# Optimization experiments

Measured on AMD Instinct MI355X. Metric: run time of the kernel, lower is better.

## Reference

```python
import jax, jax.numpy as jnp
from jax import lax
import numpy as np

K = 31      # avg_pool2d kernel_size
PAD = 15    # avg_pool2d padding
EPS = 1.0
GAMMA = 5.0


def _box_avg(x):
    # Separable 31x31 box filter, stride 1, zero padding 15,
    # count_include_pad=True (PyTorch default) -> always divide by K*K.
    s = lax.reduce_window(x, 0.0, lax.add, (1, 1, K, 1), (1, 1, 1, 1),
                          [(0, 0), (0, 0), (PAD, PAD), (0, 0)])
    s = lax.reduce_window(s, 0.0, lax.add, (1, 1, 1, K), (1, 1, 1, 1),
                          [(0, 0), (0, 0), (0, 0), (PAD, PAD)])
    return s / (K * K)


def setup_inputs() -> dict:
    key = jax.random.key(0)
    k1, k2 = jax.random.split(key)
    shape = (64, 1, 512, 512)  # [B, C, H, W]
    inp = jax.random.uniform(k1, shape, dtype=jnp.float32)
    tgt = jax.random.uniform(k2, shape, dtype=jnp.float32)
    return {"input": inp, "target": tgt}


def reference(input, target):
    weight = 1.0 + GAMMA * jnp.abs(_box_avg(target) - target)
    intersection = jnp.sum(input * target * weight)
    denom = jnp.sum(input * weight) + jnp.sum(target * weight)
    dice = (2.0 * intersection + EPS) / (denom + EPS)
    return 1.0 - dice
```

## Files before the change

### kernel.cpp

```cpp
#include <hip/hip_runtime.h>
#include <hip/hip_bf16.h>


#define BATCH 64
#define H     512
#define W     512
#define PADR  15
#define RBAND 32
#define RING  38
#define NBLK  (BATCH * (H / RBAND))

static __device__ __forceinline__ unsigned pack2(float e, float o) {
    __hip_bfloat162 h = __float22bfloat162_rn(make_float2(e, o));
    unsigned u; __builtin_memcpy(&u, &h, 4); return u;
}
static __device__ __forceinline__ float2 unpk(unsigned u) {
    return make_float2(__uint_as_float(u << 16),
                       __uint_as_float(u & 0xffff0000u));
}

__global__ __launch_bounds__(256, 4) void fused_kernel(const float* __restrict__ tgt,
                                                       const float* __restrict__ inp,
                                                       float4* __restrict__ partials) {
    const int tid  = threadIdx.x;
    const int lane = tid & 63;
    const int wv   = tid >> 6;
    const int blk  = blockIdx.x;
    const int band = blk & 15;
    const int b    = blk >> 4;
    const int R0   = band * RBAND;
    const float* timg = tgt + (size_t)b * H * W;
    const float* iimg = inp + (size_t)b * H * W;

    __shared__ __align__(16) unsigned ring[RING * 256];

    const int col0 = lane * 8;
    const int ofs  = lane * 4;

    for (int k = 0; k < 10; ++k) {
        const int r_off = wv + 4 * k;
        if (r_off < RING) {
            const int row = R0 - 15 + r_off;
            float4 v0 = make_float4(0.f, 0.f, 0.f, 0.f), v1 = v0;
            if (row >= 0) {
                v0 = *(const float4*)(timg + (size_t)row * W + col0);
                v1 = *(const float4*)(timg + (size_t)row * W + col0 + 4);
            }
            uint4 u;
            u.x = pack2(v0.x, v0.y); u.y = pack2(v0.z, v0.w);
            u.z = pack2(v1.x, v1.y); u.w = pack2(v1.z, v1.w);
            *(uint4*)&ring[((row + RING) % RING) * 256 + ofs] = u;
        }
    }
    __syncthreads();

    const float mL1 = (lane >= 1) ? 1.f : 0.f;
    const float mR1 = (lane <= 62) ? 1.f : 0.f;
    const float mL2 = (lane >= 2) ? 1.f : 0.f;
    const float mR2 = (lane <= 61) ? 1.f : 0.f;

    float vr[8];
    #pragma unroll
    for (int k = 0; k < 8; ++k) vr[k] = 0.f;
    #pragma unroll
    for (int jj = -PADR; jj <= PADR; ++jj) {
        const int rr = R0 + wv + jj;
        const uint4 c = *(const uint4*)&ring[((rr + RING) % RING) * 256 + ofs];
        const float2 e0 = unpk(c.x), e1 = unpk(c.y), e2 = unpk(c.z), e3 = unpk(c.w);
        vr[0] += e0.x; vr[1] += e0.y; vr[2] += e1.x; vr[3] += e1.y;
        vr[4] += e2.x; vr[5] += e2.y; vr[6] += e3.x; vr[7] += e3.y;
    }

    const float inv = 1.0f / 961.0f;
    float aI = 0.f, aA = 0.f, aB = 0.f;

    for (int j = 0; j < 8; ++j) {
        const int h = R0 + 4 * j + wv;

        float4 pf0 = make_float4(0.f, 0.f, 0.f, 0.f), pf1 = pf0;
        const int prow = R0 + 4 * j + 23 + wv;
        if (j < 7 && prow < H) {
            pf0 = *(const float4*)(timg + (size_t)prow * W + col0);
            pf1 = *(const float4*)(timg + (size_t)prow * W + col0 + 4);
        }
        const float4 i0 = *(const float4*)(iimg + (size_t)h * W + col0);
        const float4 i1 = *(const float4*)(iimg + (size_t)h * W + col0 + 4);

        const uint4 tc = *(const uint4*)&ring[(h % RING) * 256 + ofs];

        uint4 ua[4], us[4];
        if (j < 7) {
            #pragma unroll
            for (int q = 0; q < 4; ++q) {
                const int ar = h + 16 + q;
                ua[q] = (ar < H) ? *(const uint4*)&ring[(ar % RING) * 256 + ofs]
                                 : make_uint4(0u, 0u, 0u, 0u);
                us[q] = *(const uint4*)&ring[(((h - 15 + q) + RING) % RING) * 256 + ofs];
            }
        }

        const float p1 = vr[0];
        const float p2 = p1 + vr[1];
        const float p3 = p2 + vr[2];
        const float p4 = p3 + vr[3];
        const float p5 = p4 + vr[4];
        const float p6 = p5 + vr[5];
        const float p7 = p6 + vr[6];
        const float s  = p7 + vr[7];
        const float f1 = s - p1, f2 = s - p2, f3 = s - p3, f4 = s - p4;
        const float f5 = s - p5, f6 = s - p6, f7 = s - p7;

        const float sL1 = __shfl_up(s, 1, 64);
        const float sR1 = __shfl_down(s, 1, 64);
        const float g1 = __shfl_up(f1, 2, 64);
        const float g2 = __shfl_up(f2, 2, 64);
        const float g3 = __shfl_up(f3, 2, 64);
        const float g4 = __shfl_up(f4, 2, 64);
        const float g5 = __shfl_up(f5, 2, 64);
        const float g6 = __shfl_up(f6, 2, 64);
        const float g7 = __shfl_up(f7, 2, 64);
        const float q1 = __shfl_down(p1, 2, 64);
        const float q2 = __shfl_down(p2, 2, 64);
        const float q3 = __shfl_down(p3, 2, 64);
        const float q4 = __shfl_down(p4, 2, 64);
        const float q5 = __shfl_down(p5, 2, 64);
        const float q6 = __shfl_down(p6, 2, 64);
        const float q7 = __shfl_down(p7, 2, 64);

        const float S3 = fmaf(mL1, sL1, fmaf(mR1, sR1, s));
        float win[8];
        win[0] = fmaf(mL2, g1, S3);
        win[1] = fmaf(mL2, g2, fmaf(mR2, q1, S3));
        win[2] = fmaf(mL2, g3, fmaf(mR2, q2, S3));
        win[3] = fmaf(mL2, g4, fmaf(mR2, q3, S3));
        win[4] = fmaf(mL2, g5, fmaf(mR2, q4, S3));
        win[5] = fmaf(mL2, g6, fmaf(mR2, q5, S3));
        win[6] = fmaf(mL2, g7, fmaf(mR2, q6, S3));
        win[7] = fmaf(mR2, q7, S3);

        const float2 t0 = unpk(tc.x), t1 = unpk(tc.y), t2 = unpk(tc.z), t3 = unpk(tc.w);
        const float tv[8] = {t0.x, t0.y, t1.x, t1.y, t2.x, t2.y, t3.x, t3.y};
        const float iv[8] = {i0.x, i0.y, i0.z, i0.w, i1.x, i1.y, i1.z, i1.w};

        #pragma unroll
        for (int k = 0; k < 8; ++k) {
            const float wgt = fmaf(5.0f, fabsf(fmaf(win[k], inv, -tv[k])), 1.0f);
            aI += iv[k] * tv[k] * wgt;
            aA += iv[k] * wgt;
            aB += tv[k] * wgt;
        }

        if (j < 7) {
            #pragma unroll
            for (int q = 0; q < 4; ++q) {
                const float2 a0 = unpk(ua[q].x), a1 = unpk(ua[q].y),
                             a2 = unpk(ua[q].z), a3 = unpk(ua[q].w);
                const float2 s0 = unpk(us[q].x), s1 = unpk(us[q].y),
                             s2 = unpk(us[q].z), s3 = unpk(us[q].w);
                vr[0] += a0.x - s0.x; vr[1] += a0.y - s0.y;
                vr[2] += a1.x - s1.x; vr[3] += a1.y - s1.y;
                vr[4] += a2.x - s2.x; vr[5] += a2.y - s2.y;
                vr[6] += a3.x - s3.x; vr[7] += a3.y - s3.y;
            }
        }
        __syncthreads();

        if (j < 7 && prow < H) {
            uint4 u;
            u.x = pack2(pf0.x, pf0.y); u.y = pack2(pf0.z, pf0.w);
            u.z = pack2(pf1.x, pf1.y); u.w = pack2(pf1.z, pf1.w);
            *(uint4*)&ring[(prow % RING) * 256 + ofs] = u;
        }
        __syncthreads();
    }

    #pragma unroll
    for (int off = 32; off > 0; off >>= 1) {
        aI += __shfl_down(aI, off, 64);
        aA += __shfl_down(aA, off, 64);
        aB += __shfl_down(aB, off, 64);
    }
    float* rf = (float*)ring;
    if (lane == 0) { rf[wv] = aI; rf[8 + wv] = aA; rf[16 + wv] = aB; }
    __syncthreads();
    if (tid == 0) {
        float4 o;
        o.x = rf[0] + rf[1] + rf[2] + rf[3];
        o.y = rf[8] + rf[9] + rf[10] + rf[11];
        o.z = rf[16] + rf[17] + rf[18] + rf[19];
        o.w = 0.f;
        partials[blk] = o;
    }
}

__global__ __launch_bounds__(1024) void reduce_kernel(const float4* __restrict__ partials,
                                                      float* __restrict__ out) {
    const int tid = threadIdx.x;
    const float4 v = partials[tid];
    float aI = v.x, aA = v.y, aB = v.z;
    #pragma unroll
    for (int off = 32; off > 0; off >>= 1) {
        aI += __shfl_down(aI, off, 64);
        aA += __shfl_down(aA, off, 64);
        aB += __shfl_down(aB, off, 64);
    }
    __shared__ float s[3][16];
    const int wvx = tid >> 6, ln = tid & 63;
    if (ln == 0) { s[0][wvx] = aI; s[1][wvx] = aA; s[2][wvx] = aB; }
    __syncthreads();
    if (tid == 0) {
        float I = 0.f, A = 0.f, Bv = 0.f;
        #pragma unroll
        for (int k = 0; k < 16; ++k) { I += s[0][k]; A += s[1][k]; Bv += s[2][k]; }
        out[0] = 1.0f - (2.0f * I + 1.0f) / (A + Bv + 1.0f);
    }
}

extern "C" void kernel_launch(void* const* d_in, const int* in_sizes, int n_in,
                              void* d_out, int out_size, void* d_ws, size_t ws_size,
                              hipStream_t stream) {
    const float* inp = (const float*)d_in[0];
    const float* tgt = (const float*)d_in[1];
    float* out = (float*)d_out;

    float4* partials = (float4*)d_ws;

    fused_kernel<<<NBLK, 256, 0, stream>>>(tgt, inp, partials);
    reduce_kernel<<<1, 1024, 0, stream>>>(partials, out);
}
```

Baseline: 148.2 us.

## Process two rows per iteration with a larger LDS ring to halve barriers

Each loop iteration now handles two output rows per wave: the ring buffer grows from 38 to 42 rows, two target rows are prefetched and written per step, and the pair of __syncthreads is needed only every other row. Ring indices use conditional wrap helpers instead of modulo, and a barrier is added before the final LDS reduction reuses the ring. The aim is to cut barrier and loop overhead and expose more memory-level parallelism. The cost is more registers and LDS per block, with occupancy hint lowered from 4 to 3 blocks.

```diff
diff --git a/kernel.cpp b/kernel.cpp
--- a/kernel.cpp
+++ b/kernel.cpp
@@ -7,7 +7,7 @@
 #define W     512
 #define PADR  15
 #define RBAND 32
-#define RING  38
+#define RING  42
 #define NBLK  (BATCH * (H / RBAND))
 
 static __device__ __forceinline__ unsigned pack2(float e, float o) {
@@ -18,8 +18,14 @@
     return make_float2(__uint_as_float(u << 16),
                        __uint_as_float(u & 0xffff0000u));
 }
-
-__global__ __launch_bounds__(256, 4) void fused_kernel(const float* __restrict__ tgt,
+static __device__ __forceinline__ int wrapP(int x) {
+    return x >= RING ? x - RING : x;
+}
+static __device__ __forceinline__ int wrapN(int x) {
+    return x < 0 ? x + RING : x;
+}
+
+__global__ __launch_bounds__(256, 3) void fused_kernel(const float* __restrict__ tgt,
                                                        const float* __restrict__ inp,
                                                        float4* __restrict__ partials) {
     const int tid  = threadIdx.x;
@@ -37,7 +43,7 @@
     const int col0 = lane * 8;
     const int ofs  = lane * 4;
 
-    for (int k = 0; k < 10; ++k) {
+    for (int k = 0; k < 11; ++k) {
         const int r_off = wv + 4 * k;
         if (r_off < RING) {
             const int row = R0 - 15 + r_off;
@@ -74,104 +80,185 @@
     const float inv = 1.0f / 961.0f;
     float aI = 0.f, aA = 0.f, aB = 0.f;
 
-    for (int j = 0; j < 8; ++j) {
-        const int h = R0 + 4 * j + wv;
-
-        float4 pf0 = make_float4(0.f, 0.f, 0.f, 0.f), pf1 = pf0;
-        const int prow = R0 + 4 * j + 23 + wv;
-        if (j < 7 && prow < H) {
-            pf0 = *(const float4*)(timg + (size_t)prow * W + col0);
-            pf1 = *(const float4*)(timg + (size_t)prow * W + col0 + 4);
-        }
-        const float4 i0 = *(const float4*)(iimg + (size_t)h * W + col0);
-        const float4 i1 = *(const float4*)(iimg + (size_t)h * W + col0 + 4);
-
-        const uint4 tc = *(const uint4*)&ring[(h % RING) * 256 + ofs];
-
-        uint4 ua[4], us[4];
-        if (j < 7) {
+    for (int j = 0; j < 4; ++j) {
+        const int h1 = R0 + 8 * j + wv;
+        const int h2 = h1 + 4;
+        const int s1 = h1 % RING;
+        const int s2 = wrapP(s1 + 4);
+
+        const float4 i10 = *(const float4*)(iimg + (size_t)h1 * W + col0);
+        const float4 i11 = *(const float4*)(iimg + (size_t)h1 * W + col0 + 4);
+        const float4 i20 = *(const float4*)(iimg + (size_t)h2 * W + col0);
+        const float4 i21 = *(const float4*)(iimg + (size_t)h2 * W + col0 + 4);
+
+        float4 pa0 = make_float4(0.f,0.f,0.f,0.f), pa1 = pa0, pb0 = pa0, pb1 = pa0;
+        const int prow1 = R0 + 8 * j + 27 + wv;
+        const int prow2 = prow1 + 4;
+        if (j < 3) {
+            if (prow1 < H) {
+                pa0 = *(const float4*)(timg + (size_t)prow1 * W + col0);
+                pa1 = *(const float4*)(timg + (size_t)prow1 * W + col0 + 4);
+            }
+            if (prow2 < H) {
+                pb0 = *(const float4*)(timg + (size_t)prow2 * W + col0);
+                pb1 = *(const float4*)(timg + (size_t)prow2 * W + col0 + 4);
+            }
+        }
+
+        const uint4 tc1 = *(const uint4*)&ring[s1 * 256 + ofs];
+        const uint4 tc2 = *(const uint4*)&ring[s2 * 256 + ofs];
+
+        uint4 uaA[4], usA[4], uaB[4], usB[4];
+        #pragma unroll
+        for (int q = 0; q < 4; ++q) {
+            const int arA = h1 + 16 + q;
+            uaA[q] = (arA < H) ? *(const uint4*)&ring[wrapP(s1 + 16 + q) * 256 + ofs]
+                               : make_uint4(0u,0u,0u,0u);
+            usA[q] = *(const uint4*)&ring[wrapN(s1 - 15 + q) * 256 + ofs];
+        }
+        if (j < 3) {
             #pragma unroll
             for (int q = 0; q < 4; ++q) {
-                const int ar = h + 16 + q;
-                ua[q] = (ar < H) ? *(const uint4*)&ring[(ar % RING) * 256 + ofs]
-                                 : make_uint4(0u, 0u, 0u, 0u);
-                us[q] = *(const uint4*)&ring[(((h - 15 + q) + RING) % RING) * 256 + ofs];
-            }
-        }
-
-        const float p1 = vr[0];
-        const float p2 = p1 + vr[1];
-        const float p3 = p2 + vr[2];
-        const float p4 = p3 + vr[3];
-        const float p5 = p4 + vr[4];
-        const float p6 = p5 + vr[5];
-        const float p7 = p6 + vr[6];
-        const float s  = p7 + vr[7];
-        const float f1 = s - p1, f2 = s - p2, f3 = s - p3, f4 = s - p4;
-        const float f5 = s - p5, f6 = s - p6, f7 = s - p7;
-
-        const float sL1 = __shfl_up(s, 1, 64);
-        const float sR1 = __shfl_down(s, 1, 64);
-        const float g1 = __shfl_up(f1, 2, 64);
-        const float g2 = __shfl_up(f2, 2, 64);
-        const float g3 = __shfl_up(f3, 2, 64);
-        const float g4 = __shfl_up(f4, 2, 64);
-        const float g5 = __shfl_up(f5, 2, 64);
-        const float g6 = __shfl_up(f6, 2, 64);
-        const float g7 = __shfl_up(f7, 2, 64);
-        const float q1 = __shfl_down(p1, 2, 64);
-        const float q2 = __shfl_down(p2, 2, 64);
-        const float q3 = __shfl_down(p3, 2, 64);
-        const float q4 = __shfl_down(p4, 2, 64);
-        const float q5 = __shfl_down(p5, 2, 64);
-        const float q6 = __shfl_down(p6, 2, 64);
-        const float q7 = __shfl_down(p7, 2, 64);
-
-        const float S3 = fmaf(mL1, sL1, fmaf(mR1, sR1, s));
-        float win[8];
-        win[0] = fmaf(mL2, g1, S3);
-        win[1] = fmaf(mL2, g2, fmaf(mR2, q1, S3));
-        win[2] = fmaf(mL2, g3, fmaf(mR2, q2, S3));
-        win[3] = fmaf(mL2, g4, fmaf(mR2, q3, S3));
-        win[4] = fmaf(mL2, g5, fmaf(mR2, q4, S3));
-        win[5] = fmaf(mL2, g6, fmaf(mR2, q5, S3));
-        win[6] = fmaf(mL2, g7, fmaf(mR2, q6, S3));
-        win[7] = fmaf(mR2, q7, S3);
-
-        const float2 t0 = unpk(tc.x), t1 = unpk(tc.y), t2 = unpk(tc.z), t3 = unpk(tc.w);
-        const float tv[8] = {t0.x, t0.y, t1.x, t1.y, t2.x, t2.y, t3.x, t3.y};
-        const float iv[8] = {i0.x, i0.y, i0.z, i0.w, i1.x, i1.y, i1.z, i1.w};
+                const int arB = h1 + 20 + q;
+                uaB[q] = (arB < H) ? *(const uint4*)&ring[wrapP(s1 + 20 + q) * 256 + ofs]
+                                   : make_uint4(0u,0u,0u,0u);
+                usB[q] = *(const uint4*)&ring[wrapN(s1 - 11 + q) * 256 + ofs];
+            }
+        }
+
+        {
+            const float p1 = vr[0];
+            const float p2 = p1 + vr[1];
+            const float p3 = p2 + vr[2];
+            const float p4 = p3 + vr[3];
+            const float p5 = p4 + vr[4];
+            const float p6 = p5 + vr[5];
+            const float p7 = p6 + vr[6];
+            const float s  = p7 + vr[7];
+            const float f1 = s - p1, f2 = s - p2, f3 = s - p3, f4 = s - p4;
+            const float f5 = s - p5, f6 = s - p6, f7 = s - p7;
+
+            const float sL1 = __shfl_up(s, 1, 64);
+            const float sR1 = __shfl_down(s, 1, 64);
+            const float g1 = __shfl_up(f1, 2, 64), g2 = __shfl_up(f2, 2, 64);
+            const float g3 = __shfl_up(f3, 2, 64), g4 = __shfl_up(f4, 2, 64);
+            const float g5 = __shfl_up(f5, 2, 64), g6 = __shfl_up(f6, 2, 64);
+            const float g7 = __shfl_up(f7, 2, 64);
+            const float q1 = __shfl_down(p1, 2, 64), q2 = __shfl_down(p2, 2, 64);
+            const float q3 = __shfl_down(p3, 2, 64), q4 = __shfl_down(p4, 2, 64);
+            const float q5 = __shfl_down(p5, 2, 64), q6 = __shfl_down(p6, 2, 64);
+            const float q7 = __shfl_down(p7, 2, 64);
+
+            const float S3 = fmaf(mL1, sL1, fmaf(mR1, sR1, s));
+            float win[8];
+            win[0] = fmaf(mL2, g1, S3);
+            win[1] = fmaf(mL2, g2, fmaf(mR2, q1, S3));
+            win[2] = fmaf(mL2, g3, fmaf(mR2, q2, S3));
+            win[3] = fmaf(mL2, g4, fmaf(mR2, q3, S3));
+            win[4] = fmaf(mL2, g5, fmaf(mR2, q4, S3));
+            win[5] = fmaf(mL2, g6, fmaf(mR2, q5, S3));
+            win[6] = fmaf(mL2, g7, fmaf(mR2, q6, S3));
+            win[7] = fmaf(mR2, q7, S3);
+
+            const float2 t0 = unpk(tc1.x), t1 = unpk(tc1.y),
+                         t2 = unpk(tc1.z), t3 = unpk(tc1.w);
+            const float tv[8] = {t0.x,t0.y,t1.x,t1.y,t2.x,t2.y,t3.x,t3.y};
+            const float iv[8] = {i10.x,i10.y,i10.z,i10.w,i11.x,i11.y,i11.z,i11.w};
+            #pragma unroll
+            for (int k = 0; k < 8; ++k) {
+                const float wgt = fmaf(5.0f, fabsf(fmaf(win[k], inv, -tv[k])), 1.0f);
+                aI += iv[k] * tv[k] * wgt;
+                aA += iv[k] * wgt;
+                aB += tv[k] * wgt;
+            }
+        }
 
         #pragma unroll
-        for (int k = 0; k < 8; ++k) {
-            const float wgt = fmaf(5.0f, fabsf(fmaf(win[k], inv, -tv[k])), 1.0f);
-            aI += iv[k] * tv[k] * wgt;
-            aA += iv[k] * wgt;
-            aB += tv[k] * wgt;
-        }
-
-        if (j < 7) {
+        for (int q = 0; q < 4; ++q) {
+            const float2 a0 = unpk(uaA[q].x), a1 = unpk(uaA[q].y),
+                         a2 = unpk(uaA[q].z), a3 = unpk(uaA[q].w);
+            const float2 s0 = unpk(usA[q].x), s1v = unpk(usA[q].y),
+                         s2v = unpk(usA[q].z), s3v = unpk(usA[q].w);
+            vr[0] += a0.x - s0.x;  vr[1] += a0.y - s0.y;
+            vr[2] += a1.x - s1v.x; vr[3] += a1.y - s1v.y;
+            vr[4] += a2.x - s2v.x; vr[5] += a2.y - s2v.y;
+            vr[6] += a3.x - s3v.x; vr[7] += a3.y - s3v.y;
+        }
+
+        {
+            const float p1 = vr[0];
+            const float p2 = p1 + vr[1];
+            const float p3 = p2 + vr[2];
+            const float p4 = p3 + vr[3];
+            const float p5 = p4 + vr[4];
+            const float p6 = p5 + vr[5];
+            const float p7 = p6 + vr[6];
+            const float s  = p7 + vr[7];
+            const float f1 = s - p1, f2 = s - p2, f3 = s - p3, f4 = s - p4;
+            const float f5 = s - p5, f6 = s - p6, f7 = s - p7;
+
+            const float sL1 = __shfl_up(s, 1, 64);
+            const float sR1 = __shfl_down(s, 1, 64);
+            const float g1 = __shfl_up(f1, 2, 64), g2 = __shfl_up(f2, 2, 64);
+            const float g3 = __shfl_up(f3, 2, 64), g4 = __shfl_up(f4, 2, 64);
+            const float g5 = __shfl_up(f5, 2, 64), g6 = __shfl_up(f6, 2, 64);
+            const float g7 = __shfl_up(f7, 2, 64);
+            const float q1 = __shfl_down(p1, 2, 64), q2 = __shfl_down(p2, 2, 64);
+            const float q3 = __shfl_down(p3, 2, 64), q4 = __shfl_down(p4, 2, 64);
+            const float q5 = __shfl_down(p5, 2, 64), q6 = __shfl_down(p6, 2, 64);
+            const float q7 = __shfl_down(p7, 2, 64);
+
+            const float S3 = fmaf(mL1, sL1, fmaf(mR1, sR1, s));
+            float win[8];
+            win[0] = fmaf(mL2, g1, S3);
+            win[1] = fmaf(mL2, g2, fmaf(mR2, q1, S3));
+            win[2] = fmaf(mL2, g3, fmaf(mR2, q2, S3));
+            win[3] = fmaf(mL2, g4, fmaf(mR2, q3, S3));
+            win[4] = fmaf(mL2, g5, fmaf(mR2, q4, S3));
+            win[5] = fmaf(mL2, g6, fmaf(mR2, q5, S3));
+            win[6] = fmaf(mL2, g7, fmaf(mR2, q6, S3));
+            win[7] = fmaf(mR2, q7, S3);
+
+            const float2 t0 = unpk(tc2.x), t1 = unpk(tc2.y),
+                         t2 = unpk(tc2.z), t3 = unpk(tc2.w);
+            const float tv[8] = {t0.x,t0.y,t1.x,t1.y,t2.x,t2.y,t3.x,t3.y};
+            const float iv[8] = {i20.x,i20.y,i20.z,i20.w,i21.x,i21.y,i21.z,i21.w};
+            #pragma unroll
+            for (int k = 0; k < 8; ++k) {
+                const float wgt = fmaf(5.0f, fabsf(fmaf(win[k], inv, -tv[k])), 1.0f);
+                aI += iv[k] * tv[k] * wgt;
+                aA += iv[k] * wgt;
+                aB += tv[k] * wgt;
+            }
+        }
+
+        if (j < 3) {
             #pragma unroll
             for (int q = 0; q < 4; ++q) {
-                const float2 a0 = unpk(ua[q].x), a1 = unpk(ua[q].y),
-                             a2 = unpk(ua[q].z), a3 = unpk(ua[q].w);
-                const float2 s0 = unpk(us[q].x), s1 = unpk(us[q].y),
-                             s2 = unpk(us[q].z), s3 = unpk(us[q].w);
-                vr[0] += a0.x - s0.x; vr[1] += a0.y - s0.y;
-                vr[2] += a1.x - s1.x; vr[3] += a1.y - s1.y;
-                vr[4] += a2.x - s2.x; vr[5] += a2.y - s2.y;
-                vr[6] += a3.x - s3.x; vr[7] += a3.y - s3.y;
-            }
-        }
-        __syncthreads();
-
-        if (j < 7 && prow < H) {
-            uint4 u;
-            u.x = pack2(pf0.x, pf0.y); u.y = pack2(pf0.z, pf0.w);
-            u.z = pack2(pf1.x, pf1.y); u.w = pack2(pf1.z, pf1.w);
-            *(uint4*)&ring[(prow % RING) * 256 + ofs] = u;
-        }
-        __syncthreads();
+                const float2 a0 = unpk(uaB[q].x), a1 = unpk(uaB[q].y),
+                             a2 = unpk(uaB[q].z), a3 = unpk(uaB[q].w);
+                const float2 s0 = unpk(usB[q].x), s1v = unpk(usB[q].y),
+                             s2v = unpk(usB[q].z), s3v = unpk(usB[q].w);
+                vr[0] += a0.x - s0.x;  vr[1] += a0.y - s0.y;
+                vr[2] += a1.x - s1v.x; vr[3] += a1.y - s1v.y;
+                vr[4] += a2.x - s2v.x; vr[5] += a2.y - s2v.y;
+                vr[6] += a3.x - s3v.x; vr[7] += a3.y - s3v.y;
+            }
+            __syncthreads();
+            if (prow1 < H) {
+                uint4 u;
+                u.x = pack2(pa0.x, pa0.y); u.y = pack2(pa0.z, pa0.w);
+                u.z = pack2(pa1.x, pa1.y); u.w = pack2(pa1.z, pa1.w);
+                *(uint4*)&ring[(prow1 % RING) * 256 + ofs] = u;
+            }
+            if (prow2 < H) {
+                uint4 u;
+                u.x = pack2(pb0.x, pb0.y); u.y = pack2(pb0.z, pb0.w);
+                u.z = pack2(pb1.x, pb1.y); u.w = pack2(pb1.z, pb1.w);
+                *(uint4*)&ring[(prow2 % RING) * 256 + ofs] = u;
+            }
+            __syncthreads();
+        }
     }
 
     #pragma unroll
@@ -180,6 +267,7 @@
         aA += __shfl_down(aA, off, 64);
         aB += __shfl_down(aB, off, 64);
     }
+    __syncthreads();
     float* rf = (float*)ring;
     if (lane == 0) { rf[wv] = aI; rf[8 + wv] = aA; rf[16 + wv] = aB; }
     __syncthreads();
```

After: 301.3 us. 103% more time.
